# Kernel optimization log

Measured on AMD Instinct MI355X. Metric: run time of the kernel, lower is better.

The kernel has to match this reference:

```python
import jax, jax.numpy as jnp
import numpy as np

B, N, D, P = 64, 1024, 256, 256


def setup_inputs() -> dict:
    key = jax.random.key(0)
    kx, k1, k2, k4 = jax.random.split(key, 4)
    x = jax.random.normal(kx, (B, N, D), dtype=jnp.float32)
    # weights ~ random_uniform(-0.05, 0.05) in the original; scale here is irrelevant for math
    w1 = jax.random.uniform(k1, (D, P), dtype=jnp.float32, minval=-0.05, maxval=0.05)
    w2 = jax.random.uniform(k2, (D, P), dtype=jnp.float32, minval=-0.05, maxval=0.05)
    w4 = jax.random.uniform(k4, (P, 1), dtype=jnp.float32, minval=-0.05, maxval=0.05)
    return {"x": x, "w1": w1, "w2": w2, "w4": w4}


def reference(x, w1, w2, w4):
    # x: [B, N, D] (already stacked/transposed; query_n=key_n=values=x in the original)
    q = jax.nn.sigmoid(jnp.einsum('bnd,dp->bnp', x, w1))  # [B,N,P]
    k = jax.nn.sigmoid(jnp.einsum('bnd,dp->bnp', x, w2))  # [B,N,P]
    temper = jnp.sqrt(jnp.asarray(w1.shape[1], x.dtype))
    attn = jax.nn.softmax(jnp.einsum('bnp,bmp->bnm', q, k) / temper, axis=2)  # [B,N,N]
    # dropout(0.1) in the original is inference-identity here
    out = jnp.einsum('bnm,bmd->bnd', attn, x)             # [B,N,D]
    a = jax.nn.softmax(jnp.einsum('bnd,do->bno', out, w4), axis=1)  # [B,N,1]
    sentence = jnp.sum(x * a, axis=1)                     # [B,D]
    return sentence
```

## Files before the change

kernel.cpp:

```cpp
#include <hip/hip_runtime.h>
#include <hip/hip_bf16.h>
#include <cstdint>
#include <cstddef>

constexpr int BB = 64;
constexpr int NN = 1024;
constexpr int DD = 256;
constexpr int PP = 256;

typedef short short8 __attribute__((ext_vector_type(8)));
typedef float f32x4 __attribute__((ext_vector_type(4)));

__device__ __forceinline__ unsigned short f2bf(float f) {
    union { __hip_bfloat16 h; unsigned short u; } v;
    v.h = __float2bfloat16(f);
    return v.u;
}

__device__ __forceinline__ void async_load16(void* lds, const void* g) {
    __builtin_amdgcn_global_load_lds(
        (const __attribute__((address_space(1))) unsigned int*)g,
        (__attribute__((address_space(3))) unsigned int*)lds, 16, 0, 0);
}

__device__ __forceinline__ short8 lds_frag(const unsigned short* lds, int row, int kidx) {
    uint32_t byte = (uint32_t)(row * 512) + (uint32_t)(((kidx ^ (row & 7)) & 31) << 4);
    return *reinterpret_cast<const short8*>(reinterpret_cast<const char*>(lds) + byte);
}

__global__ void prep_wt(const float* __restrict__ w1, const float* __restrict__ w2,
                        unsigned short* __restrict__ wt) {
    int j = blockIdx.x;
    int d = threadIdx.x;
    const float* w = (j < PP) ? w1 : w2;
    int jj = j & (PP - 1);
    wt[j * DD + d] = f2bf(w[d * PP + jj]);
}

__global__ __launch_bounds__(512, 4) void qk_fused(const float* __restrict__ x,
                                                   const unsigned short* __restrict__ wt,
                                                   const float* __restrict__ w4,
                                                   unsigned short* __restrict__ qb,
                                                   unsigned short* __restrict__ kb,
                                                   float* __restrict__ xv) {
    __shared__ __align__(16) unsigned short xs[128 * 256];
    const int t = threadIdx.x, wv = t >> 6, lane = t & 63, l15 = lane & 15, l4 = lane >> 4;
    const int xbase = blockIdx.x * 128;

    {
        const int row = t >> 2, cb = t & 3;
        const float* xr = x + (size_t)(xbase + row) * DD + cb * 64;
        const float* w4r = w4 + cb * 64;
        float xvp = 0.f;
        #pragma unroll
        for (int j = 0; j < 8; j++) {
            float4 a = *reinterpret_cast<const float4*>(xr + j * 8);
            float4 bq = *reinterpret_cast<const float4*>(xr + j * 8 + 4);
            float4 wa = *reinterpret_cast<const float4*>(w4r + j * 8);
            float4 wb = *reinterpret_cast<const float4*>(w4r + j * 8 + 4);
            xvp += a.x * wa.x + a.y * wa.y + a.z * wa.z + a.w * wa.w
                 + bq.x * wb.x + bq.y * wb.y + bq.z * wb.z + bq.w * wb.w;
            short8 f;
            f[0] = (short)f2bf(a.x);  f[1] = (short)f2bf(a.y);
            f[2] = (short)f2bf(a.z);  f[3] = (short)f2bf(a.w);
            f[4] = (short)f2bf(bq.x); f[5] = (short)f2bf(bq.y);
            f[6] = (short)f2bf(bq.z); f[7] = (short)f2bf(bq.w);
            int blk = cb * 8 + j;
            uint32_t byte = (uint32_t)(row * 512) + (uint32_t)((blk ^ (row & 7)) << 4);
            *reinterpret_cast<short8*>(reinterpret_cast<char*>(xs) + byte) = f;
        }
        xvp += __shfl_xor(xvp, 1);
        xvp += __shfl_xor(xvp, 2);
        if (cb == 0) xv[xbase + row] = xvp;
    }
    __syncthreads();

    for (int h = 0; h < 2; h++) {
        short8 wf[2][8];
        #pragma unroll
        for (int pt = 0; pt < 2; pt++)
            #pragma unroll
            for (int kc = 0; kc < 8; kc++)
                wf[pt][kc] = *reinterpret_cast<const short8*>(
                    wt + (size_t)(h * 256 + wv * 32 + pt * 16 + l15) * DD + kc * 32 + l4 * 8);
        unsigned short* outp = h ? kb : qb;
        for (int set = 0; set < 8; set++) {
            f32x4 acc0 = {0.f, 0.f, 0.f, 0.f};
            f32x4 acc1 = {0.f, 0.f, 0.f, 0.f};
            #pragma unroll
            for (int kc = 0; kc < 8; kc++) {
                short8 af = lds_frag(xs, set * 16 + l15, kc * 4 + l4);
                acc0 = __builtin_amdgcn_mfma_f32_16x16x32_bf16(wf[0][kc], af, acc0, 0, 0, 0);
                acc1 = __builtin_amdgcn_mfma_f32_16x16x32_bf16(wf[1][kc], af, acc1, 0, 0, 0);
            }
            ushort4 pk;
            size_t rowoff = (size_t)(xbase + set * 16 + l15) * PP + wv * 32;
            pk.x = f2bf(1.f / (1.f + __expf(-acc0[0])));
            pk.y = f2bf(1.f / (1.f + __expf(-acc0[1])));
            pk.z = f2bf(1.f / (1.f + __expf(-acc0[2])));
            pk.w = f2bf(1.f / (1.f + __expf(-acc0[3])));
            *reinterpret_cast<ushort4*>(outp + rowoff + l4 * 4) = pk;
            pk.x = f2bf(1.f / (1.f + __expf(-acc1[0])));
            pk.y = f2bf(1.f / (1.f + __expf(-acc1[1])));
            pk.z = f2bf(1.f / (1.f + __expf(-acc1[2])));
            pk.w = f2bf(1.f / (1.f + __expf(-acc1[3])));
            *reinterpret_cast<ushort4*>(outp + rowoff + 16 + l4 * 4) = pk;
        }
    }
}

__global__ __launch_bounds__(512, 2) void attn_logit(const unsigned short* __restrict__ qb,
                                                     const unsigned short* __restrict__ kb,
                                                     const float* __restrict__ xv,
                                                     float* __restrict__ numo,
                                                     float* __restrict__ deno) {
    __shared__ __align__(16) unsigned short kq[256 * 256];
    __shared__ float xvs[256];
    const int t = threadIdx.x, wv = t >> 6, lane = t & 63, l15 = lane & 15, l4 = lane >> 4;
    const int quarter = blockIdx.x, b = blockIdx.y;
    const unsigned short* kbb = kb + ((size_t)b * NN + quarter * 256) * PP;

    {
        char* dst0 = (char*)kq + wv * 16384;
        #pragma unroll
        for (int i = 0; i < 16; i++) {
            int row = wv * 32 + i * 2 + (lane >> 5);
            int blk = (lane & 31) ^ (row & 7);
            async_load16(dst0 + i * 1024, (const char*)kbb + row * 512 + blk * 16);
        }
    }
    if (t < 256) xvs[t] = xv[b * NN + quarter * 256 + t];
    __syncthreads();

    #pragma unroll 1
    for (int p = 0; p < 2; p++) {
        short8 qf[4][8];
        const int q0 = b * NN + p * 512 + wv * 64;
        #pragma unroll
        for (int s = 0; s < 4; s++) {
            const unsigned short* qrow = qb + (size_t)(q0 + s * 16 + l15) * PP;
            #pragma unroll
            for (int kc = 0; kc < 8; kc++)
                qf[s][kc] = *reinterpret_cast<const short8*>(qrow + kc * 32 + l4 * 8);
        }
        float den[4][4], num[4][4];
        #pragma unroll
        for (int s = 0; s < 4; s++)
            #pragma unroll
            for (int r = 0; r < 4; r++) { den[s][r] = 0.f; num[s][r] = 0.f; }

        for (int mc = 0; mc < 16; mc++) {
            f32x4 z = {0.f, 0.f, 0.f, 0.f};
            f32x4 a[4] = {z, z, z, z};
            #pragma unroll
            for (int kc = 0; kc < 8; kc++) {
                short8 kf = lds_frag(kq, mc * 16 + l15, kc * 4 + l4);
                a[0] = __builtin_amdgcn_mfma_f32_16x16x32_bf16(qf[0][kc], kf, a[0], 0, 0, 0);
                a[1] = __builtin_amdgcn_mfma_f32_16x16x32_bf16(qf[1][kc], kf, a[1], 0, 0, 0);
                a[2] = __builtin_amdgcn_mfma_f32_16x16x32_bf16(qf[2][kc], kf, a[2], 0, 0, 0);
                a[3] = __builtin_amdgcn_mfma_f32_16x16x32_bf16(qf[3][kc], kf, a[3], 0, 0, 0);
            }
            float xvv = xvs[mc * 16 + l15];
            #pragma unroll
            for (int s = 0; s < 4; s++)
                #pragma unroll
                for (int r = 0; r < 4; r++) {
                    float e = __expf(a[s][r] * 0.0625f);
                    den[s][r] += e;
                    num[s][r] += e * xvv;
                }
        }
        #pragma unroll
        for (int s = 0; s < 4; s++)
            #pragma unroll
            for (int r = 0; r < 4; r++) {
                #pragma unroll
                for (int off = 1; off < 16; off <<= 1) {
                    den[s][r] += __shfl_xor(den[s][r], off);
                    num[s][r] += __shfl_xor(num[s][r], off);
                }
            }
        if (l15 == 0) {
            #pragma unroll
            for (int s = 0; s < 4; s++)
                #pragma unroll
                for (int r = 0; r < 4; r++) {
                    int n = p * 512 + wv * 64 + s * 16 + l4 * 4 + r;
                    size_t o = (size_t)quarter * BB * NN + (size_t)b * NN + n;
                    numo[o] = num[s][r];
                    deno[o] = den[s][r];
                }
        }
    }
}

__global__ __launch_bounds__(256) void sent_partial(const float* __restrict__ x,
                                                    const float* __restrict__ numo,
                                                    const float* __restrict__ deno,
                                                    float* __restrict__ part) {
    __shared__ float al[64];
    __shared__ float redA[4];
    __shared__ float redB[4];
    const int b = blockIdx.x, ch = blockIdx.y;
    const int t = threadIdx.x;
    float l[4];
    #pragma unroll
    for (int i = 0; i < 4; i++) {
        int n = b * NN + t + i * 256;
        float ns = 0.f, ds = 0.f;
        #pragma unroll
        for (int q = 0; q < 4; q++) {
            ns += numo[(size_t)q * BB * NN + n];
            ds += deno[(size_t)q * BB * NN + n];
        }
        l[i] = ns / ds;
    }
    float mx = fmaxf(fmaxf(l[0], l[1]), fmaxf(l[2], l[3]));
    #pragma unroll
    for (int off = 1; off < 64; off <<= 1) mx = fmaxf(mx, __shfl_xor(mx, off));
    if ((t & 63) == 0) redA[t >> 6] = mx;
    __syncthreads();
    mx = fmaxf(fmaxf(redA[0], redA[1]), fmaxf(redA[2], redA[3]));
    float e[4], es = 0.f;
    #pragma unroll
    for (int i = 0; i < 4; i++) { e[i] = __expf(l[i] - mx); es += e[i]; }
    #pragma unroll
    for (int off = 1; off < 64; off <<= 1) es += __shfl_xor(es, off);
    if ((t & 63) == 0) redB[t >> 6] = es;
    __syncthreads();
    float inv = 1.f / (redB[0] + redB[1] + redB[2] + redB[3]);
    int ei = ch >> 2;
    float sel = (ei == 0) ? e[0] : (ei == 1) ? e[1] : (ei == 2) ? e[2] : e[3];
    if ((t >> 6) == (ch & 3)) al[t & 63] = sel * inv;
    __syncthreads();
    float acc = 0.f;
    const float* xb = x + ((size_t)b * NN + ch * 64) * DD + t;
    #pragma unroll 8
    for (int n = 0; n < 64; n++)
        acc += al[n] * xb[(size_t)n * DD];
    part[(b * 16 + ch) * DD + t] = acc;
}

__global__ void sent_final(const float* __restrict__ part, float* __restrict__ out) {
    int b = blockIdx.x, t = threadIdx.x;
    float s = 0.f;
    #pragma unroll
    for (int c = 0; c < 16; c++) s += part[(b * 16 + c) * DD + t];
    out[b * DD + t] = s;
}

extern "C" void kernel_launch(void* const* d_in, const int* in_sizes, int n_in,
                              void* d_out, int out_size, void* d_ws, size_t ws_size,
                              hipStream_t stream) {
    (void)in_sizes; (void)n_in; (void)out_size; (void)ws_size;
    const float* x  = (const float*)d_in[0];
    const float* w1 = (const float*)d_in[1];
    const float* w2 = (const float*)d_in[2];
    const float* w4 = (const float*)d_in[3];
    float* out = (float*)d_out;

    char* ws = (char*)d_ws;
    const size_t MB = 1024 * 1024;
    unsigned short* qb   = (unsigned short*)(ws);
    unsigned short* kb   = (unsigned short*)(ws + 32 * MB);
    unsigned short* wt   = (unsigned short*)(ws + 64 * MB);
    float*          xv   = (float*)(ws + 64 * MB + 256 * 1024);
    float*          num  = (float*)(ws + 64 * MB + 512 * 1024);
    float*          den  = (float*)(ws + 64 * MB + 1536 * 1024);
    float*          part = (float*)(ws);

    prep_wt<<<dim3(2 * PP), dim3(DD), 0, stream>>>(w1, w2, wt);
    qk_fused<<<dim3(BB * NN / 128), dim3(512), 0, stream>>>(x, wt, w4, qb, kb, xv);
    attn_logit<<<dim3(4, BB), dim3(512), 0, stream>>>(qb, kb, xv, num, den);
    sent_partial<<<dim3(BB, 16), dim3(256), 0, stream>>>(x, num, den, part);
    sent_final<<<dim3(BB), dim3(DD), 0, stream>>>(part, out);
}
```

Measured before the change: 113.7 us.

## Shrink qk tiles, use exp2/rcp intrinsics, remap attention blocks across XCDs

The QK projection kernel now uses 64-row tiles with 256 threads, which halves its LDS footprint, and loops over four 128-column weight slices. Sigmoid and the softmax exponent now use hardware exp2 and rcp intrinsics in place of __expf and division. The attention kernel is launched on a flat 1D grid whose block index is remapped so all four quarters of a batch land on the same XCD, and its inner loop is partially unrolled. The aim is better occupancy, L2 locality for the shared Q rows and cheaper transcendental math, at some cost in precision and with more weight-fragment reloads per row.

New measurement: 163.8 us. 1.44x slower.

```diff
diff --git a/kernel.cpp b/kernel.cpp
--- a/kernel.cpp
+++ b/kernel.cpp
@@ -11,10 +11,16 @@
 typedef short short8 __attribute__((ext_vector_type(8)));
 typedef float f32x4 __attribute__((ext_vector_type(4)));
 
+constexpr float LOG2E = 1.4426950408889634f;
+
 __device__ __forceinline__ unsigned short f2bf(float f) {
     union { __hip_bfloat16 h; unsigned short u; } v;
     v.h = __float2bfloat16(f);
     return v.u;
+}
+
+__device__ __forceinline__ float fsigmoid(float x) {
+    return __builtin_amdgcn_rcpf(1.f + __builtin_amdgcn_exp2f(x * -LOG2E));
 }
 
 __device__ __forceinline__ void async_load16(void* lds, const void* g) {
@@ -37,15 +43,15 @@
     wt[j * DD + d] = f2bf(w[d * PP + jj]);
 }
 
-__global__ __launch_bounds__(512, 4) void qk_fused(const float* __restrict__ x,
+__global__ __launch_bounds__(256, 4) void qk_fused(const float* __restrict__ x,
                                                    const unsigned short* __restrict__ wt,
                                                    const float* __restrict__ w4,
                                                    unsigned short* __restrict__ qb,
                                                    unsigned short* __restrict__ kb,
                                                    float* __restrict__ xv) {
-    __shared__ __align__(16) unsigned short xs[128 * 256];
+    __shared__ __align__(16) unsigned short xs[64 * 256];
     const int t = threadIdx.x, wv = t >> 6, lane = t & 63, l15 = lane & 15, l4 = lane >> 4;
-    const int xbase = blockIdx.x * 128;
+    const int xbase = blockIdx.x * 64;
 
     {
         const int row = t >> 2, cb = t & 3;
@@ -75,16 +81,19 @@
     }
     __syncthreads();
 
-    for (int h = 0; h < 2; h++) {
+    #pragma unroll 1
+    for (int h = 0; h < 4; h++) {
         short8 wf[2][8];
         #pragma unroll
         for (int pt = 0; pt < 2; pt++)
             #pragma unroll
             for (int kc = 0; kc < 8; kc++)
                 wf[pt][kc] = *reinterpret_cast<const short8*>(
-                    wt + (size_t)(h * 256 + wv * 32 + pt * 16 + l15) * DD + kc * 32 + l4 * 8);
-        unsigned short* outp = h ? kb : qb;
-        for (int set = 0; set < 8; set++) {
+                    wt + (size_t)(h * 128 + wv * 32 + pt * 16 + l15) * DD + kc * 32 + l4 * 8);
+        unsigned short* outp = (h < 2) ? qb : kb;
+        const int colBase = (h & 1) * 128 + wv * 32;
+        #pragma unroll
+        for (int set = 0; set < 4; set++) {
             f32x4 acc0 = {0.f, 0.f, 0.f, 0.f};
             f32x4 acc1 = {0.f, 0.f, 0.f, 0.f};
             #pragma unroll
@@ -94,16 +103,16 @@
                 acc1 = __builtin_amdgcn_mfma_f32_16x16x32_bf16(wf[1][kc], af, acc1, 0, 0, 0);
             }
             ushort4 pk;
-            size_t rowoff = (size_t)(xbase + set * 16 + l15) * PP + wv * 32;
-            pk.x = f2bf(1.f / (1.f + __expf(-acc0[0])));
-            pk.y = f2bf(1.f / (1.f + __expf(-acc0[1])));
-            pk.z = f2bf(1.f / (1.f + __expf(-acc0[2])));
-            pk.w = f2bf(1.f / (1.f + __expf(-acc0[3])));
+            size_t rowoff = (size_t)(xbase + set * 16 + l15) * PP + colBase;
+            pk.x = f2bf(fsigmoid(acc0[0]));
+            pk.y = f2bf(fsigmoid(acc0[1]));
+            pk.z = f2bf(fsigmoid(acc0[2]));
+            pk.w = f2bf(fsigmoid(acc0[3]));
             *reinterpret_cast<ushort4*>(outp + rowoff + l4 * 4) = pk;
-            pk.x = f2bf(1.f / (1.f + __expf(-acc1[0])));
-            pk.y = f2bf(1.f / (1.f + __expf(-acc1[1])));
-            pk.z = f2bf(1.f / (1.f + __expf(-acc1[2])));
-            pk.w = f2bf(1.f / (1.f + __expf(-acc1[3])));
+            pk.x = f2bf(fsigmoid(acc1[0]));
+            pk.y = f2bf(fsigmoid(acc1[1]));
+            pk.z = f2bf(fsigmoid(acc1[2]));
+            pk.w = f2bf(fsigmoid(acc1[3]));
             *reinterpret_cast<ushort4*>(outp + rowoff + 16 + l4 * 4) = pk;
         }
     }
@@ -117,7 +126,10 @@
     __shared__ __align__(16) unsigned short kq[256 * 256];
     __shared__ float xvs[256];
     const int t = threadIdx.x, wv = t >> 6, lane = t & 63, l15 = lane & 15, l4 = lane >> 4;
-    const int quarter = blockIdx.x, b = blockIdx.y;
+    const int wg = blockIdx.x;
+    const int xcd = wg & 7, r_ = wg >> 3;
+    const int quarter = r_ & 3;
+    const int b = xcd + 8 * (r_ >> 2);
     const unsigned short* kbb = kb + ((size_t)b * NN + quarter * 256) * PP;
 
     {
@@ -149,6 +161,7 @@
             #pragma unroll
             for (int r = 0; r < 4; r++) { den[s][r] = 0.f; num[s][r] = 0.f; }
 
+        #pragma unroll 4
         for (int mc = 0; mc < 16; mc++) {
             f32x4 z = {0.f, 0.f, 0.f, 0.f};
             f32x4 a[4] = {z, z, z, z};
@@ -165,7 +178,7 @@
             for (int s = 0; s < 4; s++)
                 #pragma unroll
                 for (int r = 0; r < 4; r++) {
-                    float e = __expf(a[s][r] * 0.0625f);
+                    float e = __builtin_amdgcn_exp2f(a[s][r] * (0.0625f * LOG2E));
                     den[s][r] += e;
                     num[s][r] += e * xvv;
                 }
@@ -270,8 +283,8 @@
     float*          part = (float*)(ws);
 
     prep_wt<<<dim3(2 * PP), dim3(DD), 0, stream>>>(w1, w2, wt);
-    qk_fused<<<dim3(BB * NN / 128), dim3(512), 0, stream>>>(x, wt, w4, qb, kb, xv);
-    attn_logit<<<dim3(4, BB), dim3(512), 0, stream>>>(qb, kb, xv, num, den);
+    qk_fused<<<dim3(BB * NN / 64), dim3(256), 0, stream>>>(x, wt, w4, qb, kb, xv);
+    attn_logit<<<dim3(4 * BB), dim3(512), 0, stream>>>(qb, kb, xv, num, den);
     sent_partial<<<dim3(BB, 16), dim3(256), 0, stream>>>(x, num, den, part);
     sent_final<<<dim3(BB), dim3(DD), 0, stream>>>(part, out);
 }
```
